# Performance work log

Hardware: AMD Instinct MI355X
Metric: run time of the kernel (lower is better)

Reference implementation:

```python
import jax, jax.numpy as jnp
import numpy as np

H, NH, NKV, HD, I = 4096, 32, 8, 128, 14336
B, S = 1, 2048
THETA = 500000.0
EPS = 1e-5
SCALE = HD ** -0.5


def setup_inputs() -> dict:
    key = jax.random.key(0)
    ks = jax.random.split(key, 8)
    sc = 0.02
    return {
        "positions": jnp.arange(S, dtype=jnp.int32),
        "hidden_states": jax.random.normal(ks[0], (B, S, H), jnp.float32),
        "residual": jax.random.normal(ks[1], (B, S, H), jnp.float32),
        "w_qkv": jax.random.normal(ks[2], ((NH + 2 * NKV) * HD, H), jnp.float32) * sc,
        "w_o": jax.random.normal(ks[3], (H, NH * HD), jnp.float32) * sc,
        "w_gate_up": jax.random.normal(ks[4], (2 * I, H), jnp.float32) * sc,
        "w_down": jax.random.normal(ks[5], (H, I), jnp.float32) * sc,
        "w_ln1": jnp.ones((H,), jnp.float32),
        "w_ln2": jnp.ones((H,), jnp.float32),
    }


def rmsnorm(x, w):
    xf = x.astype(jnp.float32)
    y = xf * jax.lax.rsqrt(jnp.mean(xf * xf, axis=-1, keepdims=True) + EPS)
    return (y * w).astype(x.dtype)


def apply_rope(x, positions):
    # x: [B, S, nh, HD]; neox style: rotate halves
    half = HD // 2
    inv_freq = 1.0 / (THETA ** (jnp.arange(0, half, dtype=jnp.float32) / half))
    freqs = positions.astype(jnp.float32)[:, None] * inv_freq[None, :]  # [S, half]
    cos = jnp.cos(freqs)[None, :, None, :]
    sin = jnp.sin(freqs)[None, :, None, :]
    x1, x2 = x[..., :half], x[..., half:]
    return jnp.concatenate([x1 * cos - x2 * sin, x2 * cos + x1 * sin], axis=-1)


def reference(positions, hidden_states, residual, w_qkv, w_o, w_gate_up, w_down, w_ln1, w_ln2):
    # fused add + RMSNorm (input_layernorm with residual)
    residual = hidden_states + residual
    h = rmsnorm(residual, w_ln1)

    # fused QKV projection
    qkv = jnp.einsum('bsh,oh->bso', h, w_qkv)
    q = qkv[..., : NH * HD].reshape(B, S, NH, HD)
    k = qkv[..., NH * HD: (NH + NKV) * HD].reshape(B, S, NKV, HD)
    v = qkv[..., (NH + NKV) * HD:].reshape(B, S, NKV, HD)

    q = apply_rope(q, positions)
    k = apply_rope(k, positions)

    # GQA: expand kv heads
    rep = NH // NKV
    k = jnp.repeat(k, rep, axis=2)  # [B,S,NH,HD]
    v = jnp.repeat(v, rep, axis=2)

    scores = jnp.einsum('bqhd,bkhd->bhqk', q, k) * SCALE
    causal = jnp.tril(jnp.ones((S, S), bool))
    scores = jnp.where(causal[None, None], scores, jnp.float32(-1e30))
    attn = jax.nn.softmax(scores, axis=-1)
    ctx = jnp.einsum('bhqk,bkhd->bqhd', attn, v).reshape(B, S, NH * HD)
    attn_out = jnp.einsum('bso,ho->bsh', ctx, w_o)

    # fused add + RMSNorm (post_attention_layernorm)
    residual = attn_out + residual
    h = rmsnorm(residual, w_ln2)

    # SwiGLU MLP
    gu = jnp.einsum('bsh,oh->bso', h, w_gate_up)
    gate, up = gu[..., :I], gu[..., I:]
    h = jax.nn.silu(gate) * up
    out = jnp.einsum('bsi,hi->bsh', h, w_down)
    return out, residual
```

## Files before the change

kernel.cpp:

```cpp
#include <hip/hip_runtime.h>

typedef short bf16x8 __attribute__((ext_vector_type(8)));
typedef short short4v __attribute__((ext_vector_type(4)));
typedef float f32x4 __attribute__((ext_vector_type(4)));

#define SCALE_ATTN 0.08838834764831845f

__device__ inline short f2bs(float f) {
    unsigned u = __builtin_bit_cast(unsigned, f);
    unsigned r = (u + 0x7fffu + ((u >> 16) & 1u)) >> 16;
    return (short)(unsigned short)r;
}
__device__ inline float b2f(short s) {
    unsigned u = ((unsigned)(unsigned short)s) << 16;
    return __builtin_bit_cast(float, u);
}
__device__ inline void pack_w(const float4& a, const float4& b, bf16x8& p) {
    p[0] = f2bs(a.x); p[1] = f2bs(a.y); p[2] = f2bs(a.z); p[3] = f2bs(a.w);
    p[4] = f2bs(b.x); p[5] = f2bs(b.y); p[6] = f2bs(b.z); p[7] = f2bs(b.w);
}

__global__ __launch_bounds__(256)
void wconv_kernel(const float* __restrict__ src, short* __restrict__ dst, long n8)
{
    const long stride = (long)gridDim.x << 8;
    for (long i = ((long)blockIdx.x << 8) + threadIdx.x; i < n8; i += stride) {
        const float4 a = ((const float4*)src)[i << 1];
        const float4 b = ((const float4*)src)[(i << 1) + 1];
        bf16x8 p;
        pack_w(a, b, p);
        ((bf16x8*)dst)[i] = p;
    }
}

__global__ __launch_bounds__(512)
void wconv_gu_kernel(const float* __restrict__ src, short* __restrict__ dst)
{
    const int n = blockIdx.x;
    const int t = n >> 8, r = n & 255;
    const int orig = (r < 128) ? (t * 128 + r) : (14336 + t * 128 + (r - 128));
    const float* s = src + (long)orig * 4096;
    short* d = dst + (long)n * 4096;
    const int j = threadIdx.x << 3;
    float4 a = *(const float4*)(s + j);
    float4 b = *(const float4*)(s + j + 4);
    bf16x8 p; pack_w(a, b, p);
    *(bf16x8*)(d + j) = p;
}

__global__ __launch_bounds__(256)
void add_rmsnorm_kernel(const float* __restrict__ X, const float* __restrict__ X2,
                        const float* __restrict__ Rin, const float* __restrict__ w,
                        float* __restrict__ Rout, short* __restrict__ Hout)
{
    const int tid = threadIdx.x;
    const long base = (long)blockIdx.x << 12;
    float v[16];
    float ss = 0.f;
#pragma unroll
    for (int p = 0; p < 4; ++p) {
        const int idx = (p << 10) + (tid << 2);
        float4 a = *(const float4*)(X + base + idx);
        if (X2 != nullptr) {
            float4 b = *(const float4*)(X2 + base + idx);
            a.x += b.x; a.y += b.y; a.z += b.z; a.w += b.w;
        }
        if (Rin != nullptr) {
            float4 b = *(const float4*)(Rin + base + idx);
            a.x += b.x; a.y += b.y; a.z += b.z; a.w += b.w;
        }
        v[p*4+0] = a.x; v[p*4+1] = a.y; v[p*4+2] = a.z; v[p*4+3] = a.w;
        ss += a.x*a.x + a.y*a.y + a.z*a.z + a.w*a.w;
    }
#pragma unroll
    for (int dd = 1; dd < 64; dd <<= 1) ss += __shfl_xor(ss, dd);
    __shared__ float red[4];
    if ((tid & 63) == 0) red[tid >> 6] = ss;
    __syncthreads();
    const float tot = red[0] + red[1] + red[2] + red[3];
    const float rstd = rsqrtf(tot * (1.0f / 4096.0f) + 1e-5f);
#pragma unroll
    for (int p = 0; p < 4; ++p) {
        const int idx = (p << 10) + (tid << 2);
        if (Rout != nullptr) {
            float4 b; b.x = v[p*4+0]; b.y = v[p*4+1]; b.z = v[p*4+2]; b.w = v[p*4+3];
            *(float4*)(Rout + base + idx) = b;
        }
        float4 wv4 = *(const float4*)(w + idx);
        short4v hb;
        hb[0] = f2bs(v[p*4+0] * rstd * wv4.x);
        hb[1] = f2bs(v[p*4+1] * rstd * wv4.y);
        hb[2] = f2bs(v[p*4+2] * rstd * wv4.z);
        hb[3] = f2bs(v[p*4+3] * rstd * wv4.w);
        *(short4v*)(Hout + base + idx) = hb;
    }
}

__global__ __launch_bounds__(256)
void add2_kernel(const float* __restrict__ a, const float* __restrict__ b,
                 float* __restrict__ o, long n4)
{
    const long st = (long)gridDim.x << 8;
    for (long i = ((long)blockIdx.x << 8) + threadIdx.x; i < n4; i += st) {
        float4 x = ((const float4*)a)[i];
        float4 y = ((const float4*)b)[i];
        x.x += y.x; x.y += y.y; x.z += y.z; x.w += y.w;
        ((float4*)o)[i] = x;
    }
}

#define BAR()   do { asm volatile("" ::: "memory"); __builtin_amdgcn_s_barrier(); asm volatile("" ::: "memory"); } while (0)
#define LGKM0() asm volatile("s_waitcnt lgkmcnt(0)" ::: "memory")
#define VMW(n)  asm volatile("s_waitcnt vmcnt(" #n ")" ::: "memory")

__device__ inline bf16x8 lds_frag(const short* tile, int row, int kb) {
    const int off = row * 128 + (kb ^ ((row & 7) << 4));
    return *(const bf16x8*)((const char*)tile + off);
}

__device__ inline void stage_half(const short* __restrict__ G, long grow0, long K,
                                  long k0, short* ldsHalf, int wv, int lane)
{
#pragma unroll
    for (int i = 0; i < 2; ++i) {
        short* dst = ldsHalf + ((i << 13) + (wv << 10)) / 2;
        const int off = (wv << 10) + (i << 13) + (lane << 4);
        const int r   = off >> 7;
        const int cb  = off & 127;
        const int gcb = cb ^ ((r & 7) << 4);
        const short* src = G + (grow0 + r) * K + k0 + (gcb >> 1);
        __builtin_amdgcn_global_load_lds(
            (const __attribute__((address_space(1))) void*)(const void*)src,
            (__attribute__((address_space(3))) void*)(void*)dst, 16, 0, 0);
    }
}

#define LOAD_A(T, grp) do {                                        \
    _Pragma("unroll") for (int _m = 0; _m < 4; ++_m) {             \
        const int _row = abase + (grp)*64 + _m*16 + l15;           \
        a[_m][0] = lds_frag(T, _row, l4b);                         \
        a[_m][1] = lds_frag(T, _row, 64 + l4b);                    \
    } } while (0)

#define LOAD_B(T, n0) do {                                         \
    _Pragma("unroll") for (int _n = 0; _n < 2; ++_n) {             \
        const int _row = bbase + ((n0)+_n)*16 + l15;               \
        b[(n0)+_n][0] = lds_frag(T, _row, l4b);                    \
        b[(n0)+_n][1] = lds_frag(T, _row, 64 + l4b);               \
    } } while (0)

#define MFMA16(MB, NB) do {                                                        \
    __builtin_amdgcn_s_setprio(1);                                                 \
    _Pragma("unroll") for (int _m = 0; _m < 4; ++_m)                               \
    _Pragma("unroll") for (int _n = 0; _n < 2; ++_n) {                             \
        acc[(MB)+_m][(NB)+_n] = __builtin_amdgcn_mfma_f32_16x16x32_bf16(           \
            a[_m][0], b[(NB)+_n][0], acc[(MB)+_m][(NB)+_n], 0, 0, 0);              \
        acc[(MB)+_m][(NB)+_n] = __builtin_amdgcn_mfma_f32_16x16x32_bf16(           \
            a[_m][1], b[(NB)+_n][1], acc[(MB)+_m][(NB)+_n], 0, 0, 0);              \
    }                                                                              \
    __builtin_amdgcn_s_setprio(0);                                                 \
} while (0)

template<int EPI, int KS>
__global__ __launch_bounds__(512, 2)
void gemm8(const short* __restrict__ A, const short* __restrict__ W,
           float* __restrict__ Cf, short* __restrict__ Cb,
           int N, int K)
{
    __shared__ __align__(16) short As[2][16384];
    __shared__ __align__(16) short Bs[2][16384];

    const int tid  = threadIdx.x;
    const int lane = tid & 63;
    const int wv   = tid >> 6;
    const int wm   = wv >> 2;
    const int wn   = wv & 3;
    const int l15  = lane & 15;
    const int l4b  = (lane >> 4) << 4;

    const int gx   = gridDim.x;
    const int nwg  = gx * 8 * KS;
    const int cpx  = nwg >> 3;
    const int orig = (blockIdx.z * 8 + blockIdx.y) * gx + blockIdx.x;
    const int lgc  = (orig & 7) * cpx + (orig >> 3);
    const int by   = lgc & 7;
    const int tq   = lgc >> 3;
    const int kz   = (KS == 1) ? 0 : (tq % KS);
    const int bx   = (KS == 1) ? tq : (tq / KS);

    const long row0 = (long)by << 8;
    const long col0 = (long)bx << 8;
    const int abase = wm << 7;
    const int bbase = wn << 6;

    const int  Kc    = K / KS;
    const long kbase = (long)kz * Kc;
    const int  iters = Kc >> 7;

    f32x4 acc[8][4];
#pragma unroll
    for (int i = 0; i < 8; ++i)
#pragma unroll
        for (int j = 0; j < 4; ++j) acc[i][j] = (f32x4){0.f,0.f,0.f,0.f};

    bf16x8 a[4][2], b[4][2];

    stage_half(A, row0,       K, kbase,      &As[0][0],    wv, lane);
    stage_half(A, row0 + 128, K, kbase,      &As[0][8192], wv, lane);
    stage_half(W, col0,       K, kbase,      &Bs[0][0],    wv, lane);
    stage_half(W, col0 + 128, K, kbase,      &Bs[0][8192], wv, lane);
    stage_half(A, row0,       K, kbase + 64, &As[1][0],    wv, lane);
    stage_half(A, row0 + 128, K, kbase + 64, &As[1][8192], wv, lane);
    stage_half(W, col0,       K, kbase + 64, &Bs[1][0],    wv, lane);
    stage_half(W, col0 + 128, K, kbase + 64, &Bs[1][8192], wv, lane);
    VMW(8);
    BAR();

#pragma unroll 1
    for (int it = 0; it < iters; ++it) {
        const long k2 = kbase + ((long)(2*it + 2) << 6);
        const long k3 = k2 + 64;
        const bool pf = (it + 1 < iters);

        LOAD_A(As[0], 0); LOAD_B(Bs[0], 0);
        BAR(); LGKM0(); MFMA16(0, 0); BAR();
        LOAD_B(Bs[0], 2);
        BAR(); LGKM0(); MFMA16(0, 2); BAR();
        LOAD_A(As[0], 1);
        if (pf) stage_half(W, col0, K, k2, &Bs[0][0], wv, lane);
        BAR(); LGKM0(); MFMA16(4, 0); BAR();
        if (pf) {
            stage_half(A, row0,       K, k2, &As[0][0],    wv, lane);
            stage_half(W, col0 + 128, K, k2, &Bs[0][8192], wv, lane);
        }
        VMW(6);
        BAR(); MFMA16(4, 2); BAR();

        LOAD_A(As[1], 0); LOAD_B(Bs[1], 0);
        if (pf) stage_half(A, row0 + 128, K, k2, &As[0][8192], wv, lane);
        BAR(); LGKM0(); MFMA16(0, 0); BAR();
        LOAD_B(Bs[1], 2);
        BAR(); LGKM0(); MFMA16(0, 2); BAR();
        LOAD_A(As[1], 1);
        if (pf) {
            stage_half(W, col0,       K, k3, &Bs[1][0],    wv, lane);
            stage_half(W, col0 + 128, K, k3, &Bs[1][8192], wv, lane);
        }
        BAR(); LGKM0(); MFMA16(4, 0); BAR();
        if (pf) {
            stage_half(A, row0,       K, k3, &As[1][0],    wv, lane);
            stage_half(A, row0 + 128, K, k3, &As[1][8192], wv, lane);
        }
        VMW(8);
        BAR(); MFMA16(4, 2); BAR();
    }

    if (EPI == 0) {
        float* Cfp = Cf + ((KS > 1) ? (long)kz * ((long)N << 11) : 0);
#pragma unroll
        for (int m = 0; m < 8; ++m) {
#pragma unroll
            for (int n = 0; n < 4; ++n) {
                const long gr = row0 + (wm << 7) + m*16 + ((lane >> 4) << 2);
                const long gc = col0 + (wn << 6) + n*16 + l15;
#pragma unroll
                for (int r = 0; r < 4; ++r)
                    Cfp[(gr + r) * N + gc] = acc[m][n][r];
            }
        }
    } else {
        float* eps = (float*)&As[0][0];
        const int r4 = (lane >> 4) << 2;
        const int rr = tid >> 4;
        const int cc = (tid & 15) << 3;
#pragma unroll 1
        for (int m = 0; m < 8; ++m) {
            __syncthreads();
#pragma unroll
            for (int n = 0; n < 4; ++n)
#pragma unroll
                for (int r = 0; r < 4; ++r)
                    eps[(wm*16 + r4 + r)*272 + (wn << 6) + n*16 + l15] = acc[m][n][r];
            __syncthreads();
            const float* rowp = eps + rr * 272;
            bf16x8 ov;
#pragma unroll
            for (int e = 0; e < 8; ++e) {
                const float g = rowp[cc + e];
                const float u = rowp[cc + 128 + e];
                ov[e] = f2bs(g / (1.f + __expf(-g)) * u);
            }
            const long grow = row0 + ((rr >> 4) << 7) + m*16 + (rr & 15);
            *(bf16x8*)(Cb + grow * N + (col0 >> 1) + cc) = ov;
        }
    }
}

__global__ __launch_bounds__(128)
void rope_kernel(const int* __restrict__ pos, const float* __restrict__ qkv,
                 short* __restrict__ Qo, short* __restrict__ Ko)
{
    const int h = blockIdx.x;
    const int s = blockIdx.y;
    const int d = threadIdx.x;
    const int j = d & 63;
    const float p = (float)pos[s];
    const float invf = __expf((float)j * -0.20503692895f);
    float sn, cs;
    __sincosf(p * invf, &sn, &cs);
    const long base = (long)s * 6144 + h * 128;
    const float x1 = qkv[base + j];
    const float x2 = qkv[base + 64 + j];
    const float outv = (d < 64) ? (x1 * cs - x2 * sn) : (x2 * cs + x1 * sn);
    const short ob = f2bs(outv);
    if (h < 32) Qo[(long)s * 4096 + h * 128 + d] = ob;
    else        Ko[(long)s * 1024 + (h - 32) * 128 + d] = ob;
}

__global__ __launch_bounds__(256)
void vtrans_kernel(const float* __restrict__ qkv, short* __restrict__ Vt)
{
    __shared__ short tile[64][136];
    const int tid = threadIdx.x;
    const int s0 = blockIdx.x << 6;
    const int h = blockIdx.y;
    {
        const int srow = tid >> 2;
        const int c0 = (tid & 3) << 5;
        const float* src = qkv + (long)(s0 + srow) * 6144 + 5120 + h * 128 + c0;
#pragma unroll
        for (int m = 0; m < 8; ++m) {
            float4 f = *(const float4*)(src + (m << 2));
            tile[srow][c0 + (m << 2) + 0] = f2bs(f.x);
            tile[srow][c0 + (m << 2) + 1] = f2bs(f.y);
            tile[srow][c0 + (m << 2) + 2] = f2bs(f.z);
            tile[srow][c0 + (m << 2) + 3] = f2bs(f.w);
        }
    }
    __syncthreads();
    {
        const int d = tid >> 1;
        const int sc = (tid & 1) << 5;
        short* dst = Vt + ((long)h * 128 + d) * 2048 + s0 + sc;
#pragma unroll
        for (int m = 0; m < 4; ++m) {
            bf16x8 v;
#pragma unroll
            for (int e = 0; e < 8; ++e) v[e] = tile[sc + (m << 3) + e][d];
            *(bf16x8*)(dst + (m << 3)) = v;
        }
    }
}

__global__ __launch_bounds__(256)
void flash_kernel(const short* __restrict__ Qg, const short* __restrict__ Kg,
                  const short* __restrict__ Vtg, short* __restrict__ Ctx)
{
    __shared__ short Qs[64 * 128];
    __shared__ short Ks[64 * 128];
    __shared__ short Vs[128 * 64];
    __shared__ short Ps[4 * 16 * 64];

    const int tid  = threadIdx.x;
    const int lane = tid & 63;
    const int wv   = tid >> 6;
    const int l15  = lane & 15;
    const int l4e  = (lane >> 4) << 3;
    const int qt   = blockIdx.x;
    const int head = blockIdx.y;
    const int q0   = qt << 6;
    const int kvh  = head >> 2;

    {
        const int row = tid >> 2;
        const int c0 = (tid & 3) << 5;
        const short* src = Qg + (long)(q0 + row) * 4096 + head * 128 + c0;
        const int sw = (row & 7) << 3;
#pragma unroll
        for (int m = 0; m < 4; ++m) {
            bf16x8 v = *(const bf16x8*)(src + (m << 3));
            *(bf16x8*)&Qs[row * 128 + ((c0 + (m << 3)) ^ sw)] = v;
        }
    }

    float mrow[4], lrow[4];
    f32x4 o[8];
#pragma unroll
    for (int r = 0; r < 4; ++r) { mrow[r] = -__builtin_inff(); lrow[r] = 0.f; }
#pragma unroll
    for (int d = 0; d < 8; ++d) o[d] = (f32x4){0.f,0.f,0.f,0.f};

    for (int t = 0; t <= qt; ++t) {
        const int kv0 = t << 6;
        __syncthreads();
        {
            const int row = tid >> 2;
            const int c0 = (tid & 3) << 5;
            const short* src = Kg + (long)(kv0 + row) * 1024 + kvh * 128 + c0;
            const int sw = (row & 7) << 3;
#pragma unroll
            for (int m = 0; m < 4; ++m) {
                bf16x8 v = *(const bf16x8*)(src + (m << 3));
                *(bf16x8*)&Ks[row * 128 + ((c0 + (m << 3)) ^ sw)] = v;
            }
        }
        {
            const int d = tid >> 1;
            const int c0 = (tid & 1) << 5;
            const short* src = Vtg + ((long)kvh * 128 + d) * 2048 + kv0 + c0;
            const int sw = (d & 7) << 3;
#pragma unroll
            for (int m = 0; m < 4; ++m) {
                bf16x8 v = *(const bf16x8*)(src + (m << 3));
                *(bf16x8*)&Vs[d * 64 + ((c0 + (m << 3)) ^ sw)] = v;
            }
        }
        __syncthreads();

        bf16x8 qa[4];
        {
            const int qrow = (wv << 4) + l15;
            const int sw = (qrow & 7) << 3;
#pragma unroll
            for (int kk = 0; kk < 4; ++kk)
                qa[kk] = *(const bf16x8*)&Qs[qrow * 128 + ((l4e + (kk << 5)) ^ sw)];
        }
        f32x4 sacc[4];
#pragma unroll
        for (int j = 0; j < 4; ++j) {
            sacc[j] = (f32x4){0.f,0.f,0.f,0.f};
            const int krow = (j << 4) + l15;
            const int sw = (krow & 7) << 3;
#pragma unroll
            for (int kk = 0; kk < 4; ++kk) {
                bf16x8 kb8 = *(const bf16x8*)&Ks[krow * 128 + ((l4e + (kk << 5)) ^ sw)];
                sacc[j] = __builtin_amdgcn_mfma_f32_16x16x32_bf16(qa[kk], kb8, sacc[j], 0, 0, 0);
            }
        }

#pragma unroll
        for (int ri = 0; ri < 4; ++ri) {
            const int grow = q0 + (wv << 4) + ((lane >> 4) << 2) + ri;
            float sv[4];
#pragma unroll
            for (int j = 0; j < 4; ++j) {
                float s = sacc[j][ri] * SCALE_ATTN;
                const int col = kv0 + (j << 4) + l15;
                sv[j] = (col > grow) ? -1e30f : s;
            }
            float mx = fmaxf(fmaxf(sv[0], sv[1]), fmaxf(sv[2], sv[3]));
#pragma unroll
            for (int dd = 1; dd < 16; dd <<= 1) mx = fmaxf(mx, __shfl_xor(mx, dd));
            const float mnew = fmaxf(mrow[ri], mx);
            const float alpha = __expf(mrow[ri] - mnew);
            mrow[ri] = mnew;
            float psum = 0.f;
            short pb[4];
#pragma unroll
            for (int j = 0; j < 4; ++j) {
                float p = __expf(sv[j] - mnew);
                psum += p;
                pb[j] = f2bs(p);
            }
            lrow[ri] = lrow[ri] * alpha + psum;
#pragma unroll
            for (int d = 0; d < 8; ++d) o[d][ri] *= alpha;
            const int prow = ((lane >> 4) << 2) + ri;
            const int sw = (prow & 7) << 3;
#pragma unroll
            for (int j = 0; j < 4; ++j)
                Ps[(wv << 10) + prow * 64 + ((((j << 4) + l15)) ^ sw)] = pb[j];
        }

        bf16x8 pa0, pa1;
        {
            const int prow = l15;
            const int sw = (prow & 7) << 3;
            pa0 = *(const bf16x8*)&Ps[(wv << 10) + prow * 64 + (l4e ^ sw)];
            pa1 = *(const bf16x8*)&Ps[(wv << 10) + prow * 64 + ((l4e + 32) ^ sw)];
        }
#pragma unroll
        for (int fd = 0; fd < 8; ++fd) {
            const int drow = (fd << 4) + l15;
            const int sw = (drow & 7) << 3;
            bf16x8 v0 = *(const bf16x8*)&Vs[drow * 64 + (l4e ^ sw)];
            bf16x8 v1 = *(const bf16x8*)&Vs[drow * 64 + ((l4e + 32) ^ sw)];
            o[fd] = __builtin_amdgcn_mfma_f32_16x16x32_bf16(pa0, v0, o[fd], 0, 0, 0);
            o[fd] = __builtin_amdgcn_mfma_f32_16x16x32_bf16(pa1, v1, o[fd], 0, 0, 0);
        }
    }

    float inv[4];
#pragma unroll
    for (int ri = 0; ri < 4; ++ri) {
        float ls = lrow[ri];
#pragma unroll
        for (int dd = 1; dd < 16; dd <<= 1) ls += __shfl_xor(ls, dd);
        inv[ri] = 1.0f / ls;
    }
#pragma unroll
    for (int fd = 0; fd < 8; ++fd)
#pragma unroll
        for (int ri = 0; ri < 4; ++ri) {
            const long row = q0 + (wv << 4) + ((lane >> 4) << 2) + ri;
            Ctx[row * 4096 + head * 128 + (fd << 4) + l15] = f2bs(o[fd][ri] * inv[ri]);
        }
}

extern "C" void kernel_launch(void* const* d_in, const int* in_sizes, int n_in,
                              void* d_out, int out_size, void* d_ws, size_t ws_size,
                              hipStream_t stream)
{
    const int*   positions = (const int*)d_in[0];
    const float* hidden    = (const float*)d_in[1];
    const float* residual  = (const float*)d_in[2];
    const float* w_qkv     = (const float*)d_in[3];
    const float* w_o       = (const float*)d_in[4];
    const float* w_gu      = (const float*)d_in[5];
    const float* w_down    = (const float*)d_in[6];
    const float* w_ln1     = (const float*)d_in[7];
    const float* w_ln2     = (const float*)d_in[8];

    float* out_f   = (float*)d_out;
    float* resid2  = out_f + 8388608;
    float* resid1  = out_f;

    char* wsb = (char*)d_ws;
    short* h1     = (short*)(wsb + 0);
    short* ctx    = (short*)(wsb + 0);
    float* qkvbuf = (float*)(wsb + 16777216);
    short* h2     = (short*)(wsb + 16777216);
    short* qb     = (short*)(wsb + 67108864);
    short* kb     = (short*)(wsb + 83886080);
    short* vt     = (short*)(wsb + 88080384);
    short* hm     = (short*)(wsb + 33554432);
    float* Po     = (float*)(wsb + 100663296);
    float* Pd     = (float*)(wsb + 100663296);
    short* wbuf   = (short*)(wsb + 209715200);

    add_rmsnorm_kernel<<<2048, 256, 0, stream>>>(hidden, nullptr, residual, w_ln1, resid1, h1);
    wconv_kernel<<<2048, 256, 0, stream>>>(w_qkv, wbuf, 3145728L);
    gemm8<0,1><<<dim3(24, 8, 1), 512, 0, stream>>>(h1, wbuf, qkvbuf, nullptr, 6144, 4096);
    rope_kernel<<<dim3(40, 2048), 128, 0, stream>>>(positions, qkvbuf, qb, kb);
    vtrans_kernel<<<dim3(32, 8), 256, 0, stream>>>(qkvbuf, vt);
    flash_kernel<<<dim3(32, 32), 256, 0, stream>>>(qb, kb, vt, ctx);
    wconv_kernel<<<2048, 256, 0, stream>>>(w_o, wbuf, 2097152L);
    gemm8<0,2><<<dim3(16, 8, 2), 512, 0, stream>>>(ctx, wbuf, Po, nullptr, 4096, 4096);
    add_rmsnorm_kernel<<<2048, 256, 0, stream>>>(Po, Po + 8388608, resid1, w_ln2, resid2, h2);
    wconv_gu_kernel<<<28672, 512, 0, stream>>>(w_gu, wbuf);
    gemm8<3,1><<<dim3(112, 8, 1), 512, 0, stream>>>(h2, wbuf, nullptr, hm, 14336, 4096);
    wconv_kernel<<<2048, 256, 0, stream>>>(w_down, wbuf, 7340032L);
    gemm8<0,2><<<dim3(16, 8, 2), 512, 0, stream>>>(hm, wbuf, Pd, nullptr, 4096, 14336);
    add2_kernel<<<2048, 256, 0, stream>>>(Pd, Pd + 8388608, out_f, 2097152L);
}
```

Measured before the change: 1.462 ms.

## Use nontemporal loads for streaming kernels, pad epilogue LDS stride, reorder w_o conversion

Weight-conversion and add kernels now use nontemporal loads so streamed fp32 weights and partial sums do not evict useful cache lines. The SwiGLU epilogue LDS row stride changes from 272 to 280 floats to alter bank mapping. The w_o conversion moves earlier, into a separate buffer region, so it runs before rope/flash on the same stream. Everything stays on one stream, so the reorder changes L2 state rather than creating concurrency, and the padding enlarges the epilogue scratch footprint in LDS.

New measurement: 1.447 ms. Within noise of the previous version (-1.0%).

```diff
diff --git a/kernel.cpp b/kernel.cpp
--- a/kernel.cpp
+++ b/kernel.cpp
@@ -15,9 +15,9 @@
     unsigned u = ((unsigned)(unsigned short)s) << 16;
     return __builtin_bit_cast(float, u);
 }
-__device__ inline void pack_w(const float4& a, const float4& b, bf16x8& p) {
-    p[0] = f2bs(a.x); p[1] = f2bs(a.y); p[2] = f2bs(a.z); p[3] = f2bs(a.w);
-    p[4] = f2bs(b.x); p[5] = f2bs(b.y); p[6] = f2bs(b.z); p[7] = f2bs(b.w);
+__device__ inline void pack_w4(const f32x4& a, const f32x4& b, bf16x8& p) {
+    p[0] = f2bs(a[0]); p[1] = f2bs(a[1]); p[2] = f2bs(a[2]); p[3] = f2bs(a[3]);
+    p[4] = f2bs(b[0]); p[5] = f2bs(b[1]); p[6] = f2bs(b[2]); p[7] = f2bs(b[3]);
 }
 
 __global__ __launch_bounds__(256)
@@ -25,10 +25,10 @@
 {
     const long stride = (long)gridDim.x << 8;
     for (long i = ((long)blockIdx.x << 8) + threadIdx.x; i < n8; i += stride) {
-        const float4 a = ((const float4*)src)[i << 1];
-        const float4 b = ((const float4*)src)[(i << 1) + 1];
+        const f32x4 a = __builtin_nontemporal_load(&((const f32x4*)src)[i << 1]);
+        const f32x4 b = __builtin_nontemporal_load(&((const f32x4*)src)[(i << 1) + 1]);
         bf16x8 p;
-        pack_w(a, b, p);
+        pack_w4(a, b, p);
         ((bf16x8*)dst)[i] = p;
     }
 }
@@ -42,9 +42,9 @@
     const float* s = src + (long)orig * 4096;
     short* d = dst + (long)n * 4096;
     const int j = threadIdx.x << 3;
-    float4 a = *(const float4*)(s + j);
-    float4 b = *(const float4*)(s + j + 4);
-    bf16x8 p; pack_w(a, b, p);
+    f32x4 a = __builtin_nontemporal_load((const f32x4*)(s + j));
+    f32x4 b = __builtin_nontemporal_load((const f32x4*)(s + j + 4));
+    bf16x8 p; pack_w4(a, b, p);
     *(bf16x8*)(d + j) = p;
 }
 
@@ -60,17 +60,17 @@
 #pragma unroll
     for (int p = 0; p < 4; ++p) {
         const int idx = (p << 10) + (tid << 2);
-        float4 a = *(const float4*)(X + base + idx);
+        f32x4 a = *(const f32x4*)(X + base + idx);
         if (X2 != nullptr) {
-            float4 b = *(const float4*)(X2 + base + idx);
-            a.x += b.x; a.y += b.y; a.z += b.z; a.w += b.w;
+            f32x4 b = *(const f32x4*)(X2 + base + idx);
+            a += b;
         }
         if (Rin != nullptr) {
-            float4 b = *(const float4*)(Rin + base + idx);
-            a.x += b.x; a.y += b.y; a.z += b.z; a.w += b.w;
-        }
-        v[p*4+0] = a.x; v[p*4+1] = a.y; v[p*4+2] = a.z; v[p*4+3] = a.w;
-        ss += a.x*a.x + a.y*a.y + a.z*a.z + a.w*a.w;
+            f32x4 b = *(const f32x4*)(Rin + base + idx);
+            a += b;
+        }
+        v[p*4+0] = a[0]; v[p*4+1] = a[1]; v[p*4+2] = a[2]; v[p*4+3] = a[3];
+        ss += a[0]*a[0] + a[1]*a[1] + a[2]*a[2] + a[3]*a[3];
     }
 #pragma unroll
     for (int dd = 1; dd < 64; dd <<= 1) ss += __shfl_xor(ss, dd);
@@ -83,15 +83,16 @@
     for (int p = 0; p < 4; ++p) {
         const int idx = (p << 10) + (tid << 2);
         if (Rout != nullptr) {
-            float4 b; b.x = v[p*4+0]; b.y = v[p*4+1]; b.z = v[p*4+2]; b.w = v[p*4+3];
-            *(float4*)(Rout + base + idx) = b;
-        }
-        float4 wv4 = *(const float4*)(w + idx);
+            f32x4 b;
+            b[0] = v[p*4+0]; b[1] = v[p*4+1]; b[2] = v[p*4+2]; b[3] = v[p*4+3];
+            *(f32x4*)(Rout + base + idx) = b;
+        }
+        f32x4 wv4 = *(const f32x4*)(w + idx);
         short4v hb;
-        hb[0] = f2bs(v[p*4+0] * rstd * wv4.x);
-        hb[1] = f2bs(v[p*4+1] * rstd * wv4.y);
-        hb[2] = f2bs(v[p*4+2] * rstd * wv4.z);
-        hb[3] = f2bs(v[p*4+3] * rstd * wv4.w);
+        hb[0] = f2bs(v[p*4+0] * rstd * wv4[0]);
+        hb[1] = f2bs(v[p*4+1] * rstd * wv4[1]);
+        hb[2] = f2bs(v[p*4+2] * rstd * wv4[2]);
+        hb[3] = f2bs(v[p*4+3] * rstd * wv4[3]);
         *(short4v*)(Hout + base + idx) = hb;
     }
 }
@@ -102,10 +103,10 @@
 {
     const long st = (long)gridDim.x << 8;
     for (long i = ((long)blockIdx.x << 8) + threadIdx.x; i < n4; i += st) {
-        float4 x = ((const float4*)a)[i];
-        float4 y = ((const float4*)b)[i];
-        x.x += y.x; x.y += y.y; x.z += y.z; x.w += y.w;
-        ((float4*)o)[i] = x;
+        f32x4 x = __builtin_nontemporal_load(&((const f32x4*)a)[i]);
+        f32x4 y = __builtin_nontemporal_load(&((const f32x4*)b)[i]);
+        x += y;
+        ((f32x4*)o)[i] = x;
     }
 }
 
@@ -280,9 +281,9 @@
             for (int n = 0; n < 4; ++n)
 #pragma unroll
                 for (int r = 0; r < 4; ++r)
-                    eps[(wm*16 + r4 + r)*272 + (wn << 6) + n*16 + l15] = acc[m][n][r];
+                    eps[(wm*16 + r4 + r)*280 + (wn << 6) + n*16 + l15] = acc[m][n][r];
             __syncthreads();
-            const float* rowp = eps + rr * 272;
+            const float* rowp = eps + rr * 280;
             bf16x8 ov;
 #pragma unroll
             for (int e = 0; e < 8; ++e) {
@@ -330,11 +331,11 @@
         const float* src = qkv + (long)(s0 + srow) * 6144 + 5120 + h * 128 + c0;
 #pragma unroll
         for (int m = 0; m < 8; ++m) {
-            float4 f = *(const float4*)(src + (m << 2));
-            tile[srow][c0 + (m << 2) + 0] = f2bs(f.x);
-            tile[srow][c0 + (m << 2) + 1] = f2bs(f.y);
-            tile[srow][c0 + (m << 2) + 2] = f2bs(f.z);
-            tile[srow][c0 + (m << 2) + 3] = f2bs(f.w);
+            f32x4 f = *(const f32x4*)(src + (m << 2));
+            tile[srow][c0 + (m << 2) + 0] = f2bs(f[0]);
+            tile[srow][c0 + (m << 2) + 1] = f2bs(f[1]);
+            tile[srow][c0 + (m << 2) + 2] = f2bs(f[2]);
+            tile[srow][c0 + (m << 2) + 3] = f2bs(f[3]);
         }
     }
     __syncthreads();
@@ -537,15 +538,16 @@
     float* Po     = (float*)(wsb + 100663296);
     float* Pd     = (float*)(wsb + 100663296);
     short* wbuf   = (short*)(wsb + 209715200);
+    short* wbuf_o = wbuf + 25165824;
 
     add_rmsnorm_kernel<<<2048, 256, 0, stream>>>(hidden, nullptr, residual, w_ln1, resid1, h1);
     wconv_kernel<<<2048, 256, 0, stream>>>(w_qkv, wbuf, 3145728L);
     gemm8<0,1><<<dim3(24, 8, 1), 512, 0, stream>>>(h1, wbuf, qkvbuf, nullptr, 6144, 4096);
+    wconv_kernel<<<2048, 256, 0, stream>>>(w_o, wbuf_o, 2097152L);
     rope_kernel<<<dim3(40, 2048), 128, 0, stream>>>(positions, qkvbuf, qb, kb);
     vtrans_kernel<<<dim3(32, 8), 256, 0, stream>>>(qkvbuf, vt);
     flash_kernel<<<dim3(32, 32), 256, 0, stream>>>(qb, kb, vt, ctx);
-    wconv_kernel<<<2048, 256, 0, stream>>>(w_o, wbuf, 2097152L);
-    gemm8<0,2><<<dim3(16, 8, 2), 512, 0, stream>>>(ctx, wbuf, Po, nullptr, 4096, 4096);
+    gemm8<0,2><<<dim3(16, 8, 2), 512, 0, stream>>>(ctx, wbuf_o, Po, nullptr, 4096, 4096);
     add_rmsnorm_kernel<<<2048, 256, 0, stream>>>(Po, Po + 8388608, resid1, w_ln2, resid2, h2);
     wconv_gu_kernel<<<28672, 512, 0, stream>>>(w_gu, wbuf);
     gemm8<3,1><<<dim3(112, 8, 1), 512, 0, stream>>>(h2, wbuf, nullptr, hm, 14336, 4096);
```
